# Performance work log

Hardware: AMD Instinct MI355X
Metric: run time of the kernel (lower is better)

The kernel has to match this reference:

```python
import jax, jax.numpy as jnp
import numpy as np

VOCAB = 1_000_000
EMB = 50
OUT = 2
BATCH = 128
SEQ = 2000


def setup_inputs() -> dict:
    key = jax.random.key(0)
    k1, k2, k3 = jax.random.split(key, 3)
    t = jax.random.randint(k1, (BATCH, SEQ), 0, VOCAB, dtype=jnp.int64)
    embeddings = jax.random.normal(k2, (VOCAB, EMB), dtype=jnp.float32) * 0.02
    # xavier_uniform for the linear layer, as in the torch init
    limit = float(np.sqrt(6.0 / (EMB + OUT)))
    W = jax.random.uniform(k3, (OUT, EMB), dtype=jnp.float32, minval=-limit, maxval=limit)
    b = jnp.zeros((OUT,), dtype=jnp.float32)
    return {"t": t, "embeddings": embeddings, "W": W, "b": b}


def reference(t, embeddings, W, b):
    # embedding-bag style sum pooling: skip -1 padding positions
    mask = (t != -1)                                   # [B, S]
    safe_idx = jnp.where(mask, t, 0)
    gathered = embeddings[safe_idx] * mask[..., None].astype(embeddings.dtype)  # [B, S, E]
    # original divides by len(t) == batch size (kept faithfully)
    pooled = gathered.sum(axis=1) / jnp.asarray(t.shape[0], embeddings.dtype)   # [B, E]
    res = pooled @ W.T + b                             # [B, OUT]
    return jax.nn.relu(res)
```

## Files before the change

### kernel.cpp

```cpp
#include <hip/hip_runtime.h>

#define BATCH 128
#define SEQ   2000
#define EMB   50
#define OUTD  2

#define CHUNKS 25
#define RPB    (SEQ / CHUNKS)
#define TPB    256
#define WAVES  (TPB / 64)
#define GRP    32
#define NGRP   (TPB / GRP)
#define RPG    (RPB / NGRP)
#define LPR    (EMB / 2)

__global__ __launch_bounds__(TPB) void embbag_partial_kernel(
    const int* __restrict__ t,
    const float* __restrict__ emb,
    const float* __restrict__ W,
    float* __restrict__ partial)
{
    __shared__ int sIdx[RPB];
    __shared__ float2 red[WAVES];

    const int tid = threadIdx.x;
    const int c = blockIdx.x;
    const int b = blockIdx.y;

    if (tid < RPB) sIdx[tid] = t[b * SEQ + c * RPB + tid];
    __syncthreads();

    const int g = tid >> 5;
    const int j = tid & 31;

    float a0 = 0.0f, a1 = 0.0f;
    if (j < LPR) {
        const float2 w0 = *(const float2*)(W + 2 * j);
        const float2 w1 = *(const float2*)(W + EMB + 2 * j);
        const int* gi = sIdx + g * RPG;
#pragma unroll
        for (int r = 0; r < RPG; ++r) {
            const int idx = gi[r];
            const size_t off = (size_t)((idx < 0) ? 0 : idx) * EMB + 2 * j;
            float2 e = *(const float2*)(emb + off);
            if (idx < 0) { e.x = 0.0f; e.y = 0.0f; }
            a0 = fmaf(e.x, w0.x, fmaf(e.y, w0.y, a0));
            a1 = fmaf(e.x, w1.x, fmaf(e.y, w1.y, a1));
        }
    }

#pragma unroll
    for (int off = 32; off > 0; off >>= 1) {
        a0 += __shfl_down(a0, off, 64);
        a1 += __shfl_down(a1, off, 64);
    }
    const int wave = tid >> 6;
    const int lane = tid & 63;
    if (lane == 0) red[wave] = make_float2(a0, a1);
    __syncthreads();

    if (tid == 0) {
        float s0 = 0.0f, s1 = 0.0f;
#pragma unroll
        for (int w = 0; w < WAVES; ++w) { s0 += red[w].x; s1 += red[w].y; }
        float* p = partial + ((size_t)b * CHUNKS + c) * OUTD;
        p[0] = s0;
        p[1] = s1;
    }
}

__global__ __launch_bounds__(TPB) void finalize_kernel(
    const float* __restrict__ partial,
    const float* __restrict__ bias,
    float* __restrict__ out)
{
    const int i = threadIdx.x;
    if (i < BATCH * OUTD) {
        const int b = i >> 1;
        const int o = i & 1;
        float s = 0.0f;
#pragma unroll
        for (int cc = 0; cc < CHUNKS; ++cc)
            s += partial[((size_t)b * CHUNKS + cc) * OUTD + o];
        s = s * (1.0f / (float)BATCH) + bias[o];
        out[i] = fmaxf(s, 0.0f);
    }
}

extern "C" void kernel_launch(void* const* d_in, const int* in_sizes, int n_in,
                              void* d_out, int out_size, void* d_ws, size_t ws_size,
                              hipStream_t stream) {
    const int*   t    = (const int*)d_in[0];
    const float* emb  = (const float*)d_in[1];
    const float* W    = (const float*)d_in[2];
    const float* bias = (const float*)d_in[3];
    float* out        = (float*)d_out;
    float* partial    = (float*)d_ws;

    dim3 grid(CHUNKS, BATCH);
    embbag_partial_kernel<<<grid, TPB, 0, stream>>>(t, emb, W, partial);
    finalize_kernel<<<1, TPB, 0, stream>>>(partial, bias, out);
}
```

Measured before the change: 253.1 us.

## Fuse partial and finalize kernels into one block per batch row

Replaces the two-kernel chunked scheme (25 chunks per row, then a finalize kernel) with a single kernel that assigns one 512-thread block to each batch row and applies the bias and ReLU in place. This removes the second launch and the round trip of partials through workspace memory. The cost is that the grid shrinks from 3200 blocks to 128, which is fewer than the GPU's compute units. With each block serially processing 125 rows per 32-lane group, the random-gather workload may lose memory-level parallelism.

```diff
diff --git a/kernel.cpp b/kernel.cpp
--- a/kernel.cpp
+++ b/kernel.cpp
@@ -5,29 +5,27 @@
 #define EMB   50
 #define OUTD  2
 
-#define CHUNKS 25
-#define RPB    (SEQ / CHUNKS)
-#define TPB    256
+#define TPB    512
 #define WAVES  (TPB / 64)
 #define GRP    32
 #define NGRP   (TPB / GRP)
-#define RPG    (RPB / NGRP)
+#define RPG    (SEQ / NGRP)
 #define LPR    (EMB / 2)
 
-__global__ __launch_bounds__(TPB) void embbag_partial_kernel(
+__global__ __launch_bounds__(TPB) void embbag_fused_kernel(
     const int* __restrict__ t,
     const float* __restrict__ emb,
     const float* __restrict__ W,
-    float* __restrict__ partial)
+    const float* __restrict__ bias,
+    float* __restrict__ out)
 {
-    __shared__ int sIdx[RPB];
+    __shared__ int sIdx[SEQ];
     __shared__ float2 red[WAVES];
 
     const int tid = threadIdx.x;
-    const int c = blockIdx.x;
-    const int b = blockIdx.y;
+    const int b = blockIdx.x;
 
-    if (tid < RPB) sIdx[tid] = t[b * SEQ + c * RPB + tid];
+    for (int i = tid; i < SEQ; i += TPB) sIdx[i] = t[b * SEQ + i];
     __syncthreads();
 
     const int g = tid >> 5;
@@ -38,7 +36,7 @@
         const float2 w0 = *(const float2*)(W + 2 * j);
         const float2 w1 = *(const float2*)(W + EMB + 2 * j);
         const int* gi = sIdx + g * RPG;
-#pragma unroll
+#pragma unroll 5
         for (int r = 0; r < RPG; ++r) {
             const int idx = gi[r];
             const size_t off = (size_t)((idx < 0) ? 0 : idx) * EMB + 2 * j;
@@ -63,27 +61,9 @@
         float s0 = 0.0f, s1 = 0.0f;
 #pragma unroll
         for (int w = 0; w < WAVES; ++w) { s0 += red[w].x; s1 += red[w].y; }
-        float* p = partial + ((size_t)b * CHUNKS + c) * OUTD;
-        p[0] = s0;
-        p[1] = s1;
-    }
-}
-
-__global__ __launch_bounds__(TPB) void finalize_kernel(
-    const float* __restrict__ partial,
-    const float* __restrict__ bias,
-    float* __restrict__ out)
-{
-    const int i = threadIdx.x;
-    if (i < BATCH * OUTD) {
-        const int b = i >> 1;
-        const int o = i & 1;
-        float s = 0.0f;
-#pragma unroll
-        for (int cc = 0; cc < CHUNKS; ++cc)
-            s += partial[((size_t)b * CHUNKS + cc) * OUTD + o];
-        s = s * (1.0f / (float)BATCH) + bias[o];
-        out[i] = fmaxf(s, 0.0f);
+        const float inv = 1.0f / (float)BATCH;
+        out[b * OUTD + 0] = fmaxf(fmaf(s0, inv, bias[0]), 0.0f);
+        out[b * OUTD + 1] = fmaxf(fmaf(s1, inv, bias[1]), 0.0f);
     }
 }
 
@@ -95,9 +75,7 @@
     const float* W    = (const float*)d_in[2];
     const float* bias = (const float*)d_in[3];
     float* out        = (float*)d_out;
-    float* partial    = (float*)d_ws;
+    (void)d_ws; (void)ws_size;
 
-    dim3 grid(CHUNKS, BATCH);
-    embbag_partial_kernel<<<grid, TPB, 0, stream>>>(t, emb, W, partial);
-    finalize_kernel<<<1, TPB, 0, stream>>>(partial, bias, out);
+    embbag_fused_kernel<<<BATCH, TPB, 0, stream>>>(t, emb, W, bias, out);
 }
```

Result: no change. 252.8 us (-0.1%).
